# Performance work log

Hardware: AMD Instinct MI355X
Metric: run time of the kernel (lower is better)

## Reference

```python
import jax, jax.numpy as jnp
import numpy as np

N = 100000      # nodes
E = 1600000     # directed edges (avg degree 16)
IN, HID, OUT = 128, 128, 64


def setup_inputs() -> dict:
    key = jax.random.key(0)
    ks = jax.random.split(key, 6)
    x = jax.random.normal(ks[0], (N, IN), dtype=jnp.float32)
    edge_index = jax.random.randint(ks[1], (2, E), 0, N, dtype=jnp.int32)
    W1 = jax.random.normal(ks[2], (IN, HID), dtype=jnp.float32) * (1.0 / np.sqrt(IN))
    b1 = jax.random.normal(ks[3], (HID,), dtype=jnp.float32) * 0.01
    W2 = jax.random.normal(ks[4], (HID, OUT), dtype=jnp.float32) * (1.0 / np.sqrt(HID))
    b2 = jax.random.normal(ks[5], (OUT,), dtype=jnp.float32) * 0.01
    return {"x": x, "edge_index": edge_index, "W1": W1, "b1": b1, "W2": W2, "b2": b2}


def _gcn_norm(edge_index):
    # add self-loops, compute symmetric normalization deg^-1/2 A_hat deg^-1/2
    loop = jnp.arange(N, dtype=edge_index.dtype)
    row = jnp.concatenate([edge_index[0], loop])  # source
    col = jnp.concatenate([edge_index[1], loop])  # target
    deg = jax.ops.segment_sum(jnp.ones(row.shape[0], jnp.float32), col, num_segments=N)
    dinv = jnp.where(deg > 0, jax.lax.rsqrt(deg), 0.0)
    norm = dinv[row] * dinv[col]  # [E+N]
    return row, col, norm


def _gcn_conv(x, row, col, norm, W, b):
    h = x @ W                              # [N, out] dense transform first (fewer features moved)
    msg = h[row] * norm[:, None]           # gather over edges
    agg = jax.ops.segment_sum(msg, col, num_segments=N)  # scatter-add to targets
    return agg + b


def reference(x, edge_index, W1, b1, W2, b2):
    row, col, norm = _gcn_norm(edge_index)
    h = jax.nn.relu(_gcn_conv(x, row, col, norm, W1, b1))
    return _gcn_conv(h, row, col, norm, W2, b2)
```

## Files before the change

### kernel.cpp

```cpp
#include <hip/hip_runtime.h>

#define NN 100000
#define NE 1600000

#define BSH 9
#define BSZ 512
#define NBUK 196
#define CAP 12288
#define CHUNK 4096
#define EPT 16

typedef _Float16 hs8 __attribute__((ext_vector_type(8)));
typedef float f32x4 __attribute__((ext_vector_type(4)));
typedef float f32x2 __attribute__((ext_vector_type(2)));
#define MFMA16H(a, b, c) __builtin_amdgcn_mfma_f32_16x16x32_f16(a, b, c, 0, 0, 0)

static inline size_t alignup(size_t x) { return (x + 255) & ~(size_t)255; }

union h8u { uint4 q; _Float16 h[8]; };


__global__ __launch_bounds__(256) void k_prep0(int* __restrict__ gcur, int* __restrict__ gctl,
                                               const float* __restrict__ W1, _Float16* __restrict__ WT1,
                                               const float* __restrict__ W2, _Float16* __restrict__ WT2) {
  int b = blockIdx.x, t = threadIdx.x;
  if (b < 64) {
    int i = b * 256 + t;
    int k = i >> 7, c = i & 127;
    WT1[c * 128 + k] = (_Float16)W1[i];
  } else if (b < 96) {
    int i = (b - 64) * 256 + t;
    int k = i >> 6, c = i & 63;
    WT2[c * 128 + k] = (_Float16)W2[i];
  } else {
    if (t < NBUK) gcur[t] = t * CAP;
    if (t == 0) { gctl[0] = 0; gctl[16] = 0; }
  }
}


__device__ __forceinline__ void gemm128_body(const float* __restrict__ x, const _Float16* __restrict__ WT,
                                             unsigned char* __restrict__ t8, int bid) {
  int wave = threadIdx.x >> 6, lane = threadIdx.x & 63;
  int col0 = wave * 32;
  int lr = lane & 15;
  int lk = (lane >> 4) * 8;
  hs8 bfrag[2][4];
#pragma unroll
  for (int n = 0; n < 2; n++)
#pragma unroll
    for (int ks = 0; ks < 4; ks++)
      bfrag[n][ks] = *(const hs8*)&WT[(size_t)(col0 + n * 16 + lr) * 128 + ks * 32 + lk];
  int row0 = bid * 64;
#pragma unroll 1
  for (int mt = 0; mt < 4; mt++) {
    int r0 = row0 + mt * 16;
    if (r0 >= NN) return;
    const float* xr = x + (size_t)(r0 + lr) * 128 + lk;
    f32x4 acc[2] = {{0.f, 0.f, 0.f, 0.f}, {0.f, 0.f, 0.f, 0.f}};
#pragma unroll
    for (int ks = 0; ks < 4; ks++) {
      float4 a0 = *(const float4*)&xr[ks * 32];
      float4 a1 = *(const float4*)&xr[ks * 32 + 4];
      hs8 af;
      af[0] = (_Float16)a0.x; af[1] = (_Float16)a0.y;
      af[2] = (_Float16)a0.z; af[3] = (_Float16)a0.w;
      af[4] = (_Float16)a1.x; af[5] = (_Float16)a1.y;
      af[6] = (_Float16)a1.z; af[7] = (_Float16)a1.w;
      acc[0] = MFMA16H(af, bfrag[0][ks], acc[0]);
      acc[1] = MFMA16H(af, bfrag[1][ks], acc[1]);
    }
    int rbase = r0 + (lane >> 4) * 4;
#pragma unroll
    for (int n = 0; n < 2; n++)
#pragma unroll
      for (int r = 0; r < 4; r++) {
        uint e = (uint)__builtin_amdgcn_cvt_pk_fp8_f32(acc[n][r], acc[n][r], 0, false);
        t8[(size_t)(rbase + r) * 128 + col0 + n * 16 + lr] = (unsigned char)(e & 0xffu);
      }
  }
}


__global__ __launch_bounds__(256) void k_fused1(const int* __restrict__ row, const int* __restrict__ col,
                                                int* __restrict__ gcur, uint* __restrict__ pr_pack,
                                                const float* __restrict__ x, const _Float16* __restrict__ WT,
                                                unsigned char* __restrict__ t8, int nbB) {
  if ((int)blockIdx.x >= nbB) {
    gemm128_body(x, WT, t8, (int)blockIdx.x - nbB);
    return;
  }
  __shared__ int cnt[NBUK];
  int t = threadIdx.x;
  for (int i = t; i < NBUK; i += 256) cnt[i] = 0;
  __syncthreads();
  int e0 = blockIdx.x * CHUNK;
  uint rr[EPT]; int cc[EPT];
#pragma unroll
  for (int i = 0; i < EPT; i++) {
    int e = e0 + t + i * 256;
    bool ok = e < NE;
    cc[i] = ok ? col[e] : -1;
    rr[i] = ok ? (uint)row[e] : 0u;
  }
#pragma unroll
  for (int i = 0; i < EPT; i++)
    if (cc[i] >= 0) {
      uint rank = (uint)atomicAdd(&cnt[cc[i] >> BSH], 1);
      rr[i] |= rank << 17;
    }
  __syncthreads();
  for (int i = t; i < NBUK; i += 256) {
    int c = cnt[i];
    cnt[i] = c ? atomicAdd(&gcur[i], c) : 0;
  }
  __syncthreads();
#pragma unroll
  for (int i = 0; i < EPT; i++)
    if (cc[i] >= 0) {
      int p = cnt[cc[i] >> BSH] + (int)(rr[i] >> 17);
      pr_pack[p] = ((rr[i] & 0x1FFFFu) << BSH) | (uint)(cc[i] & (BSZ - 1));
    }
}


__global__ __launch_bounds__(256) void k_build(const uint* __restrict__ pr_pack, const int* __restrict__ gcur,
                                               int* __restrict__ deg, float* __restrict__ dinv,
                                               int* __restrict__ gctl, int* __restrict__ offs,
                                               uint2* __restrict__ wcsr) {
  __shared__ uint ep[CAP];
  __shared__ int dc[BSZ];
  __shared__ float dl[BSZ];
  __shared__ int loff[BSZ];
  __shared__ int cur[BSZ];
  __shared__ int tsum[256];
  __shared__ int sbase;
  int t = threadIdx.x, b = blockIdx.x;
  for (int i = t; i < BSZ; i += 256) dc[i] = 0;
  __syncthreads();
  int s = b * CAP;
  int n = min(gcur[b] - s, CAP);
  for (int i = t; i < n; i += 256) {
    uint v = pr_pack[s + i];
    ep[i] = v;
    atomicAdd(&dc[v & (BSZ - 1)], 1);
  }
  __syncthreads();
  int nb0 = b << BSH;
  for (int i = t; i < BSZ; i += 256) {
    int node = nb0 + i;
    if (node < NN) {
      int d = dc[i] + 1;
      deg[node] = d;
      float dv = rsqrtf((float)d);
      dinv[node] = dv;
      dl[i] = dv;
    } else {
      dl[i] = 0.f;
    }
  }
  __threadfence();
  __syncthreads();
  if (t == 0) {
    __hip_atomic_fetch_add(&gctl[16], 1, __ATOMIC_ACQ_REL, __HIP_MEMORY_SCOPE_AGENT);
    while (__hip_atomic_load(&gctl[16], __ATOMIC_ACQUIRE, __HIP_MEMORY_SCOPE_AGENT) < NBUK) {}
  }
  __syncthreads();
  __threadfence();
  int i0 = 2 * t, i1 = i0 + 1;
  int n0 = nb0 + i0, n1 = nb0 + i1;
  int d0 = (n0 < NN) ? dc[i0] + 1 : 0;
  int d1 = (n1 < NN) ? dc[i1] + 1 : 0;
  int v = d0 + d1;
  tsum[t] = v;
  __syncthreads();
  for (int d = 1; d < 256; d <<= 1) {
    int tmp = (t >= d) ? tsum[t - d] : 0;
    __syncthreads();
    tsum[t] += tmp;
    __syncthreads();
  }
  if (t == 255) sbase = atomicAdd(&gctl[0], tsum[255]);
  __syncthreads();
  int base = sbase + tsum[t] - v;
  loff[i0] = base;
  loff[i1] = base + d0;
  cur[i0] = 1;
  cur[i1] = 1;
  if (n0 < NN) {
    offs[n0] = base;
    wcsr[base] = make_uint2((uint)n0, __float_as_uint(dl[i0] * dl[i0]));
  }
  if (n1 < NN) {
    offs[n1] = base + d0;
    wcsr[base + d0] = make_uint2((uint)n1, __float_as_uint(dl[i1] * dl[i1]));
  }
  __syncthreads();
  for (int i = t; i < n; i += 256) {
    uint prk = ep[i];
    int li = (int)(prk & (BSZ - 1));
    uint r = prk >> BSH;
    int p = atomicAdd(&cur[li], 1);
    uint dru = __hip_atomic_load((const uint*)&dinv[r], __ATOMIC_RELAXED, __HIP_MEMORY_SCOPE_AGENT);
    wcsr[loff[li] + p] = make_uint2(r, __float_as_uint(__uint_as_float(dru) * dl[li]));
  }
}


__global__ __launch_bounds__(256) void k_gemm64(const _Float16* __restrict__ h, const _Float16* __restrict__ WT,
                                                _Float16* __restrict__ t2) {
  int wave = threadIdx.x >> 6, lane = threadIdx.x & 63;
  int col0 = wave * 16;
  int lr = lane & 15;
  int lk = (lane >> 4) * 8;
  hs8 bfrag[4];
#pragma unroll
  for (int ks = 0; ks < 4; ks++)
    bfrag[ks] = *(const hs8*)&WT[(size_t)(col0 + lr) * 128 + ks * 32 + lk];
  int row0 = blockIdx.x * 64;
#pragma unroll 1
  for (int mt = 0; mt < 4; mt++) {
    int r0 = row0 + mt * 16;
    if (r0 >= NN) return;
    const _Float16* hr = h + (size_t)(r0 + lr) * 128 + lk;
    f32x4 acc = {0.f, 0.f, 0.f, 0.f};
#pragma unroll
    for (int ks = 0; ks < 4; ks++) {
      hs8 af = *(const hs8*)&hr[ks * 32];
      acc = MFMA16H(af, bfrag[ks], acc);
    }
    int rbase = r0 + (lane >> 4) * 4;
#pragma unroll
    for (int r = 0; r < 4; r++)
      t2[(size_t)(rbase + r) * 64 + col0 + lr] = (_Float16)acc[r];
  }
}


__global__ __launch_bounds__(256) void k_agg128(const unsigned char* __restrict__ t8, const int* __restrict__ offs,
                                                const int* __restrict__ deg, const uint2* __restrict__ wcsr,
                                                const float* __restrict__ bias, _Float16* __restrict__ out) {
  int wave = threadIdx.x >> 6, lane = threadIdx.x & 63;
  int half = lane >> 5;
  int sub = (lane >> 4) & 1;
  int f = lane & 15;
  int node = blockIdx.x * 8 + wave * 2 + half;
  int beg = offs[node];
  int d = deg[node];
  const char* tb = (const char*)t8;
  float acc[8] = {};
  int trips = (d + 1) >> 1;
  uint2 e = (sub < d) ? wcsr[beg + sub] : make_uint2(0u, 0u);
#pragma unroll 1
  for (int k = 0; k < trips; k++) {
    int ns = (k + 1) * 2 + sub;
    uint2 en = (ns < d) ? wcsr[beg + ns] : make_uint2(0u, 0u);
    float s = __uint_as_float(e.y);
    uint2 u = *(const uint2*)(tb + (((size_t)e.x) << 7) + (f << 3));
    f32x2 p0 = __builtin_amdgcn_cvt_pk_f32_fp8(u.x, false);
    f32x2 p1 = __builtin_amdgcn_cvt_pk_f32_fp8(u.x, true);
    f32x2 p2 = __builtin_amdgcn_cvt_pk_f32_fp8(u.y, false);
    f32x2 p3 = __builtin_amdgcn_cvt_pk_f32_fp8(u.y, true);
    acc[0] = fmaf(p0[0], s, acc[0]);
    acc[1] = fmaf(p0[1], s, acc[1]);
    acc[2] = fmaf(p1[0], s, acc[2]);
    acc[3] = fmaf(p1[1], s, acc[3]);
    acc[4] = fmaf(p2[0], s, acc[4]);
    acc[5] = fmaf(p2[1], s, acc[5]);
    acc[6] = fmaf(p3[0], s, acc[6]);
    acc[7] = fmaf(p3[1], s, acc[7]);
    e = en;
  }
#pragma unroll
  for (int j = 0; j < 8; j++) acc[j] += __shfl_xor(acc[j], 16);
  if (sub == 0) {
    float4 b0 = *(const float4*)&bias[f * 8];
    float4 b1 = *(const float4*)&bias[f * 8 + 4];
    h8u st;
    st.h[0] = (_Float16)fmaxf(acc[0] + b0.x, 0.f);
    st.h[1] = (_Float16)fmaxf(acc[1] + b0.y, 0.f);
    st.h[2] = (_Float16)fmaxf(acc[2] + b0.z, 0.f);
    st.h[3] = (_Float16)fmaxf(acc[3] + b0.w, 0.f);
    st.h[4] = (_Float16)fmaxf(acc[4] + b1.x, 0.f);
    st.h[5] = (_Float16)fmaxf(acc[5] + b1.y, 0.f);
    st.h[6] = (_Float16)fmaxf(acc[6] + b1.z, 0.f);
    st.h[7] = (_Float16)fmaxf(acc[7] + b1.w, 0.f);
    *(uint4*)&out[(size_t)node * 128 + f * 8] = st.q;
  }
}

__global__ __launch_bounds__(256) void k_agg64(const _Float16* __restrict__ t, const int* __restrict__ offs,
                                               const int* __restrict__ deg, const uint2* __restrict__ wcsr,
                                               const float* __restrict__ bias, float* __restrict__ out) {
  int wave = threadIdx.x >> 6, lane = threadIdx.x & 63;
  int half = lane >> 5;
  int sub = (lane >> 3) & 3;
  int f8 = lane & 7;
  int node = blockIdx.x * 8 + wave * 2 + half;
  int beg = offs[node];
  int d = deg[node];
  const char* tb = (const char*)t;
  float acc[8] = {};
  int trips = (d + 3) >> 2;
  uint2 e = (sub < d) ? wcsr[beg + sub] : make_uint2(0u, 0u);
#pragma unroll 1
  for (int k = 0; k < trips; k++) {
    int ns = (k + 1) * 4 + sub;
    uint2 en = (ns < d) ? wcsr[beg + ns] : make_uint2(0u, 0u);
    float s = __uint_as_float(e.y);
    h8u u;
    u.q = *(const uint4*)(tb + (((size_t)e.x) << 7) + (f8 << 4));
    acc[0] = fmaf((float)u.h[0], s, acc[0]);
    acc[1] = fmaf((float)u.h[1], s, acc[1]);
    acc[2] = fmaf((float)u.h[2], s, acc[2]);
    acc[3] = fmaf((float)u.h[3], s, acc[3]);
    acc[4] = fmaf((float)u.h[4], s, acc[4]);
    acc[5] = fmaf((float)u.h[5], s, acc[5]);
    acc[6] = fmaf((float)u.h[6], s, acc[6]);
    acc[7] = fmaf((float)u.h[7], s, acc[7]);
    e = en;
  }
#pragma unroll
  for (int j = 0; j < 8; j++) {
    acc[j] += __shfl_xor(acc[j], 8);
    acc[j] += __shfl_xor(acc[j], 16);
  }
  if (sub == 0) {
    float4 b0 = *(const float4*)&bias[f8 * 8];
    float4 b1 = *(const float4*)&bias[f8 * 8 + 4];
    float4 o0 = make_float4(acc[0] + b0.x, acc[1] + b0.y, acc[2] + b0.z, acc[3] + b0.w);
    float4 o1 = make_float4(acc[4] + b1.x, acc[5] + b1.y, acc[6] + b1.z, acc[7] + b1.w);
    *(float4*)&out[(size_t)node * 64 + f8 * 8] = o0;
    *(float4*)&out[(size_t)node * 64 + f8 * 8 + 4] = o1;
  }
}


extern "C" void kernel_launch(void* const* d_in, const int* in_sizes, int n_in,
                              void* d_out, int out_size, void* d_ws, size_t ws_size,
                              hipStream_t stream) {
  const float* x  = (const float*)d_in[0];
  const int*   ei = (const int*)d_in[1];
  const float* W1 = (const float*)d_in[2];
  const float* b1 = (const float*)d_in[3];
  const float* W2 = (const float*)d_in[4];
  const float* b2 = (const float*)d_in[5];
  float* out = (float*)d_out;

  char* p = (char*)d_ws;
  int* deg       = (int*)p;      p += alignup((size_t)NN * 4);
  int* gcur      = (int*)p;      p += alignup((size_t)NBUK * 4);
  int* offs      = (int*)p;      p += alignup((size_t)NN * 4);
  int* gctl      = (int*)p;      p += alignup(256);
  float* dinv    = (float*)p;    p += alignup((size_t)NN * 4);
  uint2* wcsr    = (uint2*)p;    p += alignup((size_t)(NE + NN + 64) * 8);
  _Float16* WT1  = (_Float16*)p; p += alignup(128 * 128 * 2);
  _Float16* WT2  = (_Float16*)p; p += alignup(64 * 128 * 2);
  unsigned char* t8 = (unsigned char*)p; p += alignup((size_t)NN * 128);
  _Float16* t2   = (_Float16*)p; p += alignup((size_t)NN * 64 * 2);
  _Float16* h1   = (_Float16*)p; p += alignup((size_t)NN * 128 * 2);
  uint* pr_pack  = (uint*)t2;
  (void)ws_size; (void)in_sizes; (void)n_in; (void)out_size;

  const int* row = ei;
  const int* col = ei + NE;

  int nbB = (NE + CHUNK - 1) / CHUNK;
  int nbG = (NN + 63) / 64;
  int nbA = NN / 8;

  k_prep0<<<97, 256, 0, stream>>>(gcur, gctl, W1, WT1, W2, WT2);
  k_fused1<<<nbB + nbG, 256, 0, stream>>>(row, col, gcur, pr_pack, x, WT1, t8, nbB);
  k_build<<<NBUK, 256, 0, stream>>>(pr_pack, gcur, deg, dinv, gctl, offs, wcsr);
  k_agg128<<<nbA, 256, 0, stream>>>(t8, offs, deg, wcsr, b1, h1);
  k_gemm64<<<nbG, 256, 0, stream>>>(h1, WT2, t2);
  k_agg64<<<nbA, 256, 0, stream>>>(t2, offs, deg, wcsr, b2, out);
}
```

Baseline: 208.5 us.

## Fold symmetric norm into GEMM outputs and aggregate over index-only CSR

After: 199.5 us. 1.05x faster.

```diff
diff --git a/kernel.cpp b/kernel.cpp
--- a/kernel.cpp
+++ b/kernel.cpp
@@ -20,27 +20,85 @@
 union h8u { uint4 q; _Float16 h[8]; };
 
 
-__global__ __launch_bounds__(256) void k_prep0(int* __restrict__ gcur, int* __restrict__ gctl,
-                                               const float* __restrict__ W1, _Float16* __restrict__ WT1,
-                                               const float* __restrict__ W2, _Float16* __restrict__ WT2) {
-  int b = blockIdx.x, t = threadIdx.x;
-  if (b < 64) {
-    int i = b * 256 + t;
-    int k = i >> 7, c = i & 127;
-    WT1[c * 128 + k] = (_Float16)W1[i];
-  } else if (b < 96) {
-    int i = (b - 64) * 256 + t;
-    int k = i >> 6, c = i & 63;
-    WT2[c * 128 + k] = (_Float16)W2[i];
-  } else {
-    if (t < NBUK) gcur[t] = t * CAP;
-    if (t == 0) { gctl[0] = 0; gctl[16] = 0; }
+__global__ __launch_bounds__(256) void k_fused0(const int* __restrict__ row, const int* __restrict__ col,
+                                                int* __restrict__ gcur, uint* __restrict__ pr_pack,
+                                                const float* __restrict__ W1, _Float16* __restrict__ WT1,
+                                                const float* __restrict__ W2, _Float16* __restrict__ WT2,
+                                                unsigned char* __restrict__ t8, int nbB) {
+  int b = (int)blockIdx.x, t = threadIdx.x;
+  if (b >= nbB) {
+    int w = b - nbB;
+    if (w < 64) {
+      int i = w * 256 + t;
+      int k = i >> 7, c = i & 127;
+      WT1[c * 128 + k] = (_Float16)W1[i];
+    } else if (w < 96) {
+      int i = (w - 64) * 256 + t;
+      int k = i >> 6, c = i & 63;
+      WT2[c * 128 + k] = (_Float16)W2[i];
+    } else {
+      if (t < 32) ((uint*)(t8 + (size_t)NN * 128))[t] = 0u;
+    }
+    return;
+  }
+  __shared__ int cnt[NBUK];
+  for (int i = t; i < NBUK; i += 256) cnt[i] = 0;
+  __syncthreads();
+  int e0 = b * CHUNK;
+  uint rr[EPT]; int cc[EPT];
+#pragma unroll
+  for (int i = 0; i < EPT; i++) {
+    int e = e0 + t + i * 256;
+    bool ok = e < NE;
+    cc[i] = ok ? col[e] : -1;
+    rr[i] = ok ? (uint)row[e] : 0u;
+  }
+#pragma unroll
+  for (int i = 0; i < EPT; i++)
+    if (cc[i] >= 0) {
+      uint rank = (uint)atomicAdd(&cnt[cc[i] >> BSH], 1);
+      rr[i] |= rank << 17;
+    }
+  __syncthreads();
+  for (int i = t; i < NBUK; i += 256) {
+    int c = cnt[i];
+    cnt[i] = c ? (i * CAP + atomicAdd(&gcur[i], c)) : 0;
+  }
+  __syncthreads();
+#pragma unroll
+  for (int i = 0; i < EPT; i++)
+    if (cc[i] >= 0) {
+      int p = cnt[cc[i] >> BSH] + (int)(rr[i] >> 17);
+      pr_pack[p] = ((rr[i] & 0x1FFFFu) << BSH) | (uint)(cc[i] & (BSZ - 1));
+    }
+}
+
+
+__global__ __launch_bounds__(256) void k_bdeg(const uint* __restrict__ pr_pack, const int* __restrict__ gcur,
+                                              int* __restrict__ deg, float* __restrict__ dinv) {
+  __shared__ int dc[BSZ];
+  int t = threadIdx.x, b = blockIdx.x;
+  for (int i = t; i < BSZ; i += 256) dc[i] = 0;
+  __syncthreads();
+  int s = b * CAP;
+  int n = min(gcur[b], CAP);
+  for (int i = t; i < n; i += 256) atomicAdd(&dc[pr_pack[s + i] & (BSZ - 1)], 1);
+  __syncthreads();
+  int nb0 = b << BSH;
+  for (int i = t; i < BSZ; i += 256) {
+    int node = nb0 + i;
+    if (node < NN) {
+      int d = dc[i] + 1;
+      deg[node] = d;
+      dinv[node] = rsqrtf((float)d);
+    }
   }
 }
 
 
 __device__ __forceinline__ void gemm128_body(const float* __restrict__ x, const _Float16* __restrict__ WT,
-                                             unsigned char* __restrict__ t8, int bid) {
+                                             const float* __restrict__ dinv, unsigned char* __restrict__ t8,
+                                             int bid) {
   int wave = threadIdx.x >> 6, lane = threadIdx.x & 63;
   int col0 = wave * 32;
   int lr = lane & 15;
@@ -72,105 +130,38 @@
     }
     int rbase = r0 + (lane >> 4) * 4;
 #pragma unroll
-    for (int n = 0; n < 2; n++)
-#pragma unroll
-      for (int r = 0; r < 4; r++) {
-        uint e = (uint)__builtin_amdgcn_cvt_pk_fp8_f32(acc[n][r], acc[n][r], 0, false);
+    for (int r = 0; r < 4; r++) {
+      float dv = dinv[rbase + r];
+#pragma unroll
+      for (int n = 0; n < 2; n++) {
+        float v = acc[n][r] * dv;
+        uint e = (uint)__builtin_amdgcn_cvt_pk_fp8_f32(v, v, 0, false);
         t8[(size_t)(rbase + r) * 128 + col0 + n * 16 + lr] = (unsigned char)(e & 0xffu);
       }
-  }
-}
-
-
-__global__ __launch_bounds__(256) void k_fused1(const int* __restrict__ row, const int* __restrict__ col,
-                                                int* __restrict__ gcur, uint* __restrict__ pr_pack,
+    }
+  }
+}
+
+
+__global__ __launch_bounds__(256) void k_fused2(const uint* __restrict__ pr_pack, const int* __restrict__ gcur,
+                                                const int* __restrict__ deg, int* __restrict__ gctl,
+                                                int* __restrict__ offs, int* __restrict__ csr,
                                                 const float* __restrict__ x, const _Float16* __restrict__ WT,
-                                                unsigned char* __restrict__ t8, int nbB) {
-  if ((int)blockIdx.x >= nbB) {
-    gemm128_body(x, WT, t8, (int)blockIdx.x - nbB);
+                                                const float* __restrict__ dinv, unsigned char* __restrict__ t8) {
+  if ((int)blockIdx.x >= NBUK) {
+    gemm128_body(x, WT, dinv, t8, (int)blockIdx.x - NBUK);
     return;
   }
-  __shared__ int cnt[NBUK];
-  int t = threadIdx.x;
-  for (int i = t; i < NBUK; i += 256) cnt[i] = 0;
-  __syncthreads();
-  int e0 = blockIdx.x * CHUNK;
-  uint rr[EPT]; int cc[EPT];
-#pragma unroll
-  for (int i = 0; i < EPT; i++) {
-    int e = e0 + t + i * 256;
-    bool ok = e < NE;
-    cc[i] = ok ? col[e] : -1;
-    rr[i] = ok ? (uint)row[e] : 0u;
-  }
-#pragma unroll
-  for (int i = 0; i < EPT; i++)
-    if (cc[i] >= 0) {
-      uint rank = (uint)atomicAdd(&cnt[cc[i] >> BSH], 1);
-      rr[i] |= rank << 17;
-    }
-  __syncthreads();
-  for (int i = t; i < NBUK; i += 256) {
-    int c = cnt[i];
-    cnt[i] = c ? atomicAdd(&gcur[i], c) : 0;
-  }
-  __syncthreads();
-#pragma unroll
-  for (int i = 0; i < EPT; i++)
-    if (cc[i] >= 0) {
-      int p = cnt[cc[i] >> BSH] + (int)(rr[i] >> 17);
-      pr_pack[p] = ((rr[i] & 0x1FFFFu) << BSH) | (uint)(cc[i] & (BSZ - 1));
-    }
-}
-
-
-__global__ __launch_bounds__(256) void k_build(const uint* __restrict__ pr_pack, const int* __restrict__ gcur,
-                                               int* __restrict__ deg, float* __restrict__ dinv,
-                                               int* __restrict__ gctl, int* __restrict__ offs,
-                                               uint2* __restrict__ wcsr) {
-  __shared__ uint ep[CAP];
-  __shared__ int dc[BSZ];
-  __shared__ float dl[BSZ];
   __shared__ int loff[BSZ];
   __shared__ int cur[BSZ];
   __shared__ int tsum[256];
   __shared__ int sbase;
   int t = threadIdx.x, b = blockIdx.x;
-  for (int i = t; i < BSZ; i += 256) dc[i] = 0;
-  __syncthreads();
-  int s = b * CAP;
-  int n = min(gcur[b] - s, CAP);
-  for (int i = t; i < n; i += 256) {
-    uint v = pr_pack[s + i];
-    ep[i] = v;
-    atomicAdd(&dc[v & (BSZ - 1)], 1);
-  }
-  __syncthreads();
   int nb0 = b << BSH;
-  for (int i = t; i < BSZ; i += 256) {
-    int node = nb0 + i;
-    if (node < NN) {
-      int d = dc[i] + 1;
-      deg[node] = d;
-      float dv = rsqrtf((float)d);
-      dinv[node] = dv;
-      dl[i] = dv;
-    } else {
-      dl[i] = 0.f;
-    }
-  }
-  __threadfence();
-  __syncthreads();
-  if (t == 0) {
-    __hip_atomic_fetch_add(&gctl[16], 1, __ATOMIC_ACQ_REL, __HIP_MEMORY_SCOPE_AGENT);
-    while (__hip_atomic_load(&gctl[16], __ATOMIC_ACQUIRE, __HIP_MEMORY_SCOPE_AGENT) < NBUK) {}
-  }
-  __syncthreads();
-  __threadfence();
   int i0 = 2 * t, i1 = i0 + 1;
   int n0 = nb0 + i0, n1 = nb0 + i1;
-  int d0 = (n0 < NN) ? dc[i0] + 1 : 0;
-  int d1 = (n1 < NN) ? dc[i1] + 1 : 0;
+  int d0 = (n0 < NN) ? deg[n0] : 0;
+  int d1 = (n1 < NN) ? deg[n1] : 0;
   int v = d0 + d1;
   tsum[t] = v;
   __syncthreads();
@@ -187,28 +178,27 @@
   loff[i1] = base + d0;
   cur[i0] = 1;
   cur[i1] = 1;
-  if (n0 < NN) {
-    offs[n0] = base;
-    wcsr[base] = make_uint2((uint)n0, __float_as_uint(dl[i0] * dl[i0]));
-  }
-  if (n1 < NN) {
-    offs[n1] = base + d0;
-    wcsr[base + d0] = make_uint2((uint)n1, __float_as_uint(dl[i1] * dl[i1]));
-  }
-  __syncthreads();
+  if (n0 < NN) { offs[n0] = base;      csr[base] = n0; }
+  if (n1 < NN) { offs[n1] = base + d0; csr[base + d0] = n1; }
+  __syncthreads();
+  int s = b * CAP;
+  int n = min(gcur[b], CAP);
   for (int i = t; i < n; i += 256) {
-    uint prk = ep[i];
+    uint prk = pr_pack[s + i];
     int li = (int)(prk & (BSZ - 1));
-    uint r = prk >> BSH;
     int p = atomicAdd(&cur[li], 1);
-    uint dru = __hip_atomic_load((const uint*)&dinv[r], __ATOMIC_RELAXED, __HIP_MEMORY_SCOPE_AGENT);
-    wcsr[loff[li] + p] = make_uint2(r, __float_as_uint(__uint_as_float(dru) * dl[li]));
+    csr[loff[li] + p] = (int)(prk >> BSH);
   }
 }
 
 
 __global__ __launch_bounds__(256) void k_gemm64(const _Float16* __restrict__ h, const _Float16* __restrict__ WT,
-                                                _Float16* __restrict__ t2) {
+                                                const float* __restrict__ dinv, _Float16* __restrict__ t2,
+                                                int nbG) {
+  if ((int)blockIdx.x >= nbG) {
+    if (threadIdx.x < 32) ((uint*)(t2 + (size_t)NN * 64))[threadIdx.x] = 0u;
+    return;
+  }
   int wave = threadIdx.x >> 6, lane = threadIdx.x & 63;
   int col0 = wave * 16;
   int lr = lane & 15;
@@ -232,14 +222,15 @@
     int rbase = r0 + (lane >> 4) * 4;
 #pragma unroll
     for (int r = 0; r < 4; r++)
-      t2[(size_t)(rbase + r) * 64 + col0 + lr] = (_Float16)acc[r];
+      t2[(size_t)(rbase + r) * 64 + col0 + lr] = (_Float16)(acc[r] * dinv[rbase + r]);
   }
 }
 
 
 __global__ __launch_bounds__(256) void k_agg128(const unsigned char* __restrict__ t8, const int* __restrict__ offs,
-                                                const int* __restrict__ deg, const uint2* __restrict__ wcsr,
-                                                const float* __restrict__ bias, _Float16* __restrict__ out) {
+                                                const int* __restrict__ deg, const int* __restrict__ csr,
+                                                const float* __restrict__ dinv, const float* __restrict__ bias,
+                                                _Float16* __restrict__ out) {
   int wave = threadIdx.x >> 6, lane = threadIdx.x & 63;
   int half = lane >> 5;
   int sub = (lane >> 4) & 1;
@@ -250,48 +241,45 @@
   const char* tb = (const char*)t8;
   float acc[8] = {};
   int trips = (d + 1) >> 1;
-  uint2 e = (sub < d) ? wcsr[beg + sub] : make_uint2(0u, 0u);
+  int r = (sub < d) ? csr[beg + sub] : NN;
 #pragma unroll 1
   for (int k = 0; k < trips; k++) {
     int ns = (k + 1) * 2 + sub;
-    uint2 en = (ns < d) ? wcsr[beg + ns] : make_uint2(0u, 0u);
-    float s = __uint_as_float(e.y);
-    uint2 u = *(const uint2*)(tb + (((size_t)e.x) << 7) + (f << 3));
+    int rn = (ns < d) ? csr[beg + ns] : NN;
+    uint2 u = *(const uint2*)(tb + (((size_t)(uint)r) << 7) + (f << 3));
     f32x2 p0 = __builtin_amdgcn_cvt_pk_f32_fp8(u.x, false);
     f32x2 p1 = __builtin_amdgcn_cvt_pk_f32_fp8(u.x, true);
     f32x2 p2 = __builtin_amdgcn_cvt_pk_f32_fp8(u.y, false);
     f32x2 p3 = __builtin_amdgcn_cvt_pk_f32_fp8(u.y, true);
-    acc[0] = fmaf(p0[0], s, acc[0]);
-    acc[1] = fmaf(p0[1], s, acc[1]);
-    acc[2] = fmaf(p1[0], s, acc[2]);
-    acc[3] = fmaf(p1[1], s, acc[3]);
-    acc[4] = fmaf(p2[0], s, acc[4]);
-    acc[5] = fmaf(p2[1], s, acc[5]);
-    acc[6] = fmaf(p3[0], s, acc[6]);
-    acc[7] = fmaf(p3[1], s, acc[7]);
-    e = en;
+    acc[0] += p0[0]; acc[1] += p0[1];
+    acc[2] += p1[0]; acc[3] += p1[1];
+    acc[4] += p2[0]; acc[5] += p2[1];
+    acc[6] += p3[0]; acc[7] += p3[1];
+    r = rn;
   }
 #pragma unroll
   for (int j = 0; j < 8; j++) acc[j] += __shfl_xor(acc[j], 16);
   if (sub == 0) {
+    float dv = dinv[node];
     float4 b0 = *(const float4*)&bias[f * 8];
     float4 b1 = *(const float4*)&bias[f * 8 + 4];
     h8u st;
-    st.h[0] = (_Float16)fmaxf(acc[0] + b0.x, 0.f);
-    st.h[1] = (_Float16)fmaxf(acc[1] + b0.y, 0.f);
-    st.h[2] = (_Float16)fmaxf(acc[2] + b0.z, 0.f);
-    st.h[3] = (_Float16)fmaxf(acc[3] + b0.w, 0.f);
-    st.h[4] = (_Float16)fmaxf(acc[4] + b1.x, 0.f);
-    st.h[5] = (_Float16)fmaxf(acc[5] + b1.y, 0.f);
-    st.h[6] = (_Float16)fmaxf(acc[6] + b1.z, 0.f);
-    st.h[7] = (_Float16)fmaxf(acc[7] + b1.w, 0.f);
+    st.h[0] = (_Float16)fmaxf(fmaf(acc[0], dv, b0.x), 0.f);
+    st.h[1] = (_Float16)fmaxf(fmaf(acc[1], dv, b0.y), 0.f);
+    st.h[2] = (_Float16)fmaxf(fmaf(acc[2], dv, b0.z), 0.f);
+    st.h[3] = (_Float16)fmaxf(fmaf(acc[3], dv, b0.w), 0.f);
+    st.h[4] = (_Float16)fmaxf(fmaf(acc[4], dv, b1.x), 0.f);
+    st.h[5] = (_Float16)fmaxf(fmaf(acc[5], dv, b1.y), 0.f);
+    st.h[6] = (_Float16)fmaxf(fmaf(acc[6], dv, b1.z), 0.f);
+    st.h[7] = (_Float16)fmaxf(fmaf(acc[7], dv, b1.w), 0.f);
     *(uint4*)&out[(size_t)node * 128 + f * 8] = st.q;
   }
 }
 
 __global__ __launch_bounds__(256) void k_agg64(const _Float16* __restrict__ t, const int* __restrict__ offs,
-                                               const int* __restrict__ deg, const uint2* __restrict__ wcsr,
-                                               const float* __restrict__ bias, float* __restrict__ out) {
+                                               const int* __restrict__ deg, const int* __restrict__ csr,
+                                               const float* __restrict__ dinv, const float* __restrict__ bias,
+                                               float* __restrict__ out) {
   int wave = threadIdx.x >> 6, lane = threadIdx.x & 63;
   int half = lane >> 5;
   int sub = (lane >> 3) & 3;
@@ -302,23 +290,22 @@
   const char* tb = (const char*)t;
   float acc[8] = {};
   int trips = (d + 3) >> 2;
-  uint2 e = (sub < d) ? wcsr[beg + sub] : make_uint2(0u, 0u);
+  int r = (sub < d) ? csr[beg + sub] : NN;
 #pragma unroll 1
   for (int k = 0; k < trips; k++) {
     int ns = (k + 1) * 4 + sub;
-    uint2 en = (ns < d) ? wcsr[beg + ns] : make_uint2(0u, 0u);
-    float s = __uint_as_float(e.y);
+    int rn = (ns < d) ? csr[beg + ns] : NN;
     h8u u;
-    u.q = *(const uint4*)(tb + (((size_t)e.x) << 7) + (f8 << 4));
-    acc[0] = fmaf((float)u.h[0], s, acc[0]);
-    acc[1] = fmaf((float)u.h[1], s, acc[1]);
-    acc[2] = fmaf((float)u.h[2], s, acc[2]);
-    acc[3] = fmaf((float)u.h[3], s, acc[3]);
-    acc[4] = fmaf((float)u.h[4], s, acc[4]);
-    acc[5] = fmaf((float)u.h[5], s, acc[5]);
-    acc[6] = fmaf((float)u.h[6], s, acc[6]);
-    acc[7] = fmaf((float)u.h[7], s, acc[7]);
-    e = en;
+    u.q = *(const uint4*)(tb + (((size_t)(uint)r) << 7) + (f8 << 4));
+    acc[0] += (float)u.h[0];
+    acc[1] += (float)u.h[1];
+    acc[2] += (float)u.h[2];
+    acc[3] += (float)u.h[3];
+    acc[4] += (float)u.h[4];
+    acc[5] += (float)u.h[5];
+    acc[6] += (float)u.h[6];
+    acc[7] += (float)u.h[7];
+    r = rn;
   }
 #pragma unroll
   for (int j = 0; j < 8; j++) {
@@ -326,10 +313,13 @@
     acc[j] += __shfl_xor(acc[j], 16);
   }
   if (sub == 0) {
+    float dv = dinv[node];
     float4 b0 = *(const float4*)&bias[f8 * 8];
     float4 b1 = *(const float4*)&bias[f8 * 8 + 4];
-    float4 o0 = make_float4(acc[0] + b0.x, acc[1] + b0.y, acc[2] + b0.z, acc[3] + b0.w);
-    float4 o1 = make_float4(acc[4] + b1.x, acc[5] + b1.y, acc[6] + b1.z, acc[7] + b1.w);
+    float4 o0 = make_float4(fmaf(acc[0], dv, b0.x), fmaf(acc[1], dv, b0.y),
+                            fmaf(acc[2], dv, b0.z), fmaf(acc[3], dv, b0.w));
+    float4 o1 = make_float4(fmaf(acc[4], dv, b1.x), fmaf(acc[5], dv, b1.y),
+                            fmaf(acc[6], dv, b1.z), fmaf(acc[7], dv, b1.w));
     *(float4*)&out[(size_t)node * 64 + f8 * 8] = o0;
     *(float4*)&out[(size_t)node * 64 + f8 * 8 + 4] = o1;
   }
@@ -348,16 +338,16 @@
   float* out = (float*)d_out;
 
   char* p = (char*)d_ws;
+  int* gcur      = (int*)p;      p += alignup((size_t)NBUK * 4);
+  int* gctl      = (int*)p;      p += alignup(256);
   int* deg       = (int*)p;      p += alignup((size_t)NN * 4);
-  int* gcur      = (int*)p;      p += alignup((size_t)NBUK * 4);
   int* offs      = (int*)p;      p += alignup((size_t)NN * 4);
-  int* gctl      = (int*)p;      p += alignup(256);
   float* dinv    = (float*)p;    p += alignup((size_t)NN * 4);
-  uint2* wcsr    = (uint2*)p;    p += alignup((size_t)(NE + NN + 64) * 8);
+  int* csr       = (int*)p;      p += alignup((size_t)(NE + NN + 64) * 4);
   _Float16* WT1  = (_Float16*)p; p += alignup(128 * 128 * 2);
   _Float16* WT2  = (_Float16*)p; p += alignup(64 * 128 * 2);
-  unsigned char* t8 = (unsigned char*)p; p += alignup((size_t)NN * 128);
-  _Float16* t2   = (_Float16*)p; p += alignup((size_t)NN * 64 * 2);
+  unsigned char* t8 = (unsigned char*)p; p += alignup((size_t)(NN + 1) * 128);
+  _Float16* t2   = (_Float16*)p; p += alignup((size_t)(NN + 1) * 64 * 2);
   _Float16* h1   = (_Float16*)p; p += alignup((size_t)NN * 128 * 2);
   uint* pr_pack  = (uint*)t2;
   (void)ws_size; (void)in_sizes; (void)n_in; (void)out_size;
@@ -369,10 +359,11 @@
   int nbG = (NN + 63) / 64;
   int nbA = NN / 8;
 
-  k_prep0<<<97, 256, 0, stream>>>(gcur, gctl, W1, WT1, W2, WT2);
-  k_fused1<<<nbB + nbG, 256, 0, stream>>>(row, col, gcur, pr_pack, x, WT1, t8, nbB);
-  k_build<<<NBUK, 256, 0, stream>>>(pr_pack, gcur, deg, dinv, gctl, offs, wcsr);
-  k_agg128<<<nbA, 256, 0, stream>>>(t8, offs, deg, wcsr, b1, h1);
-  k_gemm64<<<nbG, 256, 0, stream>>>(h1, WT2, t2);
-  k_agg64<<<nbA, 256, 0, stream>>>(t2, offs, deg, wcsr, b2, out);
-}
+  hipMemsetAsync(gcur, 0, alignup((size_t)NBUK * 4) + 256, stream);
+  k_fused0<<<nbB + 97, 256, 0, stream>>>(row, col, gcur, pr_pack, W1, WT1, W2, WT2, t8, nbB);
+  k_bdeg<<<NBUK, 256, 0, stream>>>(pr_pack, gcur, deg, dinv);
+  k_fused2<<<NBUK + nbG, 256, 0, stream>>>(pr_pack, gcur, deg, gctl, offs, csr, x, WT1, dinv, t8);
+  k_agg128<<<nbA, 256, 0, stream>>>(t8, offs, deg, csr, dinv, b1, h1);
+  k_gemm64<<<nbG + 1, 256, 0, stream>>>(h1, WT2, dinv, t2, nbG);
+  k_agg64<<<nbA, 256, 0, stream>>>(t2, offs, deg, csr, dinv, b2, out);
+}
```
